# Kernel optimization log

Measured on AMD Instinct MI355X. Metric: run time of the kernel, lower is better.

## Reference

```python
import jax, jax.numpy as jnp
import numpy as np

B, S, D_MODEL = 1, 2048, 2048
H, KVH = 16, 4
HD = D_MODEL // H          # 128
N_REP = H // KVH           # 4 (GQA)
WINDOW = 1024              # window_size=(WINDOW-1, 0): self + 1023 past tokens
CLIP = 8.0
THETA = 500000.0
EPS = 1e-6
SCALE = 1.0 / (HD ** 0.5)


def rms_norm(x, w):
    # per-head RMSNorm over last dim (head_dim)
    var = jnp.mean(jnp.square(x), axis=-1, keepdims=True)
    return x * jax.lax.rsqrt(var + EPS) * w


def rope_tables():
    inv_freq = 1.0 / (THETA ** (jnp.arange(0, HD, 2, dtype=jnp.float32) / HD))
    pos = jnp.arange(S, dtype=jnp.float32)
    freqs = pos[:, None] * inv_freq[None, :]          # [S, HD/2]
    emb = jnp.concatenate([freqs, freqs], axis=-1)    # [S, HD]
    return jnp.cos(emb), jnp.sin(emb)


def rotate_half(x):
    x1, x2 = x[..., : HD // 2], x[..., HD // 2 :]
    return jnp.concatenate([-x2, x1], axis=-1)


def apply_rope(x, cos, sin):
    # x: [B, S, h, HD]; cos/sin: [S, HD]
    return x * cos[None, :, None, :] + rotate_half(x) * sin[None, :, None, :]


def setup_inputs() -> dict:
    key = jax.random.key(0)
    ks = jax.random.split(key, 7)
    w = lambda k, shape: jax.random.normal(k, shape, jnp.float32) * 0.02
    return {
        "x": jax.random.normal(ks[0], (B, S, D_MODEL), jnp.float32),
        "w_q": w(ks[1], (D_MODEL, D_MODEL)),
        "w_k": w(ks[2], (KVH * HD, D_MODEL)),
        "w_v": w(ks[3], (KVH * HD, D_MODEL)),
        "w_out": w(ks[4], (D_MODEL, D_MODEL)),
        "q_norm_w": jnp.ones((HD,), jnp.float32),
        "k_norm_w": jnp.ones((HD,), jnp.float32),
        "sinks": jax.random.normal(ks[5], (H,), jnp.float32),
    }


def reference(x, w_q, w_k, w_v, w_out, q_norm_w, k_norm_w, sinks):
    # fused QKV projection + clip
    q = jnp.clip(x @ w_q.T, -CLIP, CLIP).reshape(B, S, H, HD)
    k = jnp.clip(x @ w_k.T, -CLIP, CLIP).reshape(B, S, KVH, HD)
    v = jnp.clip(x @ w_v.T, -CLIP, CLIP).reshape(B, S, KVH, HD)

    # per-head qk RMSNorm, then RoPE
    q = rms_norm(q, q_norm_w)
    k = rms_norm(k, k_norm_w)
    cos, sin = rope_tables()
    q = apply_rope(q, cos, sin)
    k = apply_rope(k, cos, sin)

    # GQA: repeat_interleave kv heads
    k = jnp.repeat(k, N_REP, axis=2)  # [B, S, H, HD]
    v = jnp.repeat(v, N_REP, axis=2)

    # sliding-window causal attention with a learned per-head sink logit
    logits = jnp.einsum("bqhd,bkhd->bhqk", q, k) * SCALE  # [B, H, S, S]
    qi = jnp.arange(S)[:, None]
    ki = jnp.arange(S)[None, :]
    mask = (ki <= qi) & (ki > qi - WINDOW)                # causal + window
    logits = jnp.where(mask[None, None, :, :], logits, -jnp.inf)

    # sink token: always-visible extra logit sinks[h] with zero value vector
    sink_col = jnp.broadcast_to(sinks[None, :, None, None], (B, H, S, 1))
    full = jnp.concatenate([logits, sink_col], axis=-1)   # [B, H, S, S+1]
    probs = jax.nn.softmax(full, axis=-1)

    att = jnp.einsum("bhqk,bkhd->bqhd", probs[..., :S], v)  # sink value is 0
    return att.reshape(B, S, D_MODEL) @ w_out.T
```

## Files before the change

### kernel.cpp

```cpp
#include <hip/hip_runtime.h>
#include <hip/hip_bf16.h>
#include <math.h>

#define S_LEN 2048
#define DMODEL 2048
#define NH 16
#define NKVH 4
#define HDIM 128
#define WINDOW 1024

typedef __bf16 bf16;
typedef __bf16 bf16x8 __attribute__((ext_vector_type(8)));
typedef __bf16 bf16x4 __attribute__((ext_vector_type(4)));
typedef float floatx4 __attribute__((ext_vector_type(4)));

static __device__ __forceinline__ bf16x8 load_bf8(const bf16* p) {
    return *reinterpret_cast<const bf16x8*>(p);
}

static __device__ __forceinline__ void async16(const bf16* g, bf16* l) {
    __builtin_amdgcn_global_load_lds(
        (const __attribute__((address_space(1))) void*)g,
        (__attribute__((address_space(3))) void*)l, 16, 0, 0);
}

__global__ __launch_bounds__(256) void convert_kernel(
    const float* __restrict__ x, const float* __restrict__ wq,
    const float* __restrict__ wk, const float* __restrict__ wv,
    const float* __restrict__ wo,
    bf16* __restrict__ xb, bf16* __restrict__ wqb, bf16* __restrict__ wkb,
    bf16* __restrict__ wvb, bf16* __restrict__ wob) {
    for (int i = blockIdx.x * blockDim.x + threadIdx.x; i < 3670016;
         i += gridDim.x * blockDim.x) {
        const float* src; bf16* dst; int off;
        if      (i < 1048576) { src = x;  dst = xb;  off = i; }
        else if (i < 2097152) { src = wq; dst = wqb; off = i - 1048576; }
        else if (i < 2359296) { src = wk; dst = wkb; off = i - 2097152; }
        else if (i < 2621440) { src = wv; dst = wvb; off = i - 2359296; }
        else                  { src = wo; dst = wob; off = i - 2621440; }
        float4 v = reinterpret_cast<const float4*>(src)[off];
        union { bf16 b[4]; ushort4 u; } t;
        t.b[0] = (bf16)v.x; t.b[1] = (bf16)v.y;
        t.b[2] = (bf16)v.z; t.b[3] = (bf16)v.w;
        reinterpret_cast<ushort4*>(dst)[off] = t.u;
    }
}

#define GEMM_BODY()                                                            \
    __shared__ __align__(16) bf16 smem[2 * (64 + 128) * 64];        \
    int tid = threadIdx.x;                                                     \
    int lane = tid & 63, wid = tid >> 6;                                       \
    int l15 = lane & 15, quad = lane >> 4;                                     \
    int rlocal = lane >> 3;                                                    \
    int scol = ((lane & 7) ^ rlocal) * 8;                                      \
    const bf16* gA = A + (size_t)(m0 + wid * 16 + rlocal) * K + scol;          \
    const bf16* gB = B + (size_t)(n0 + wid * 32 + rlocal) * K + scol;          \
    int ldsOfA = (wid * 16) * 64;                                               \
    int ldsOfB = (wid * 32) * 64;                                               \
    floatx4 acc[2][4];                                                         \
    _Pragma("unroll") for (int mi = 0; mi < 2; ++mi)                           \
        _Pragma("unroll") for (int ni = 0; ni < 4; ++ni)                       \
            acc[mi][ni] = floatx4{0.f, 0.f, 0.f, 0.f};                         \
    int mb = (wid & 1) * 32, nb = (wid >> 1) * 64;                             \
    _Pragma("unroll") for (int j = 0; j < 2; ++j)                              \
        async16(gA + (size_t)(j * 8) * K, smem + ldsOfA + j * 512);            \
    _Pragma("unroll") for (int j = 0; j < 4; ++j)                              \
        async16(gB + (size_t)(j * 8) * K, smem + 8192 + ldsOfB + j * 512);     \
    int buf = 0;                                                               \
    for (int k0 = 0; k0 < K; k0 += 64) {                                       \
        __syncthreads();                                                       \
        if (k0 + 64 < K) {                                                     \
            int nof = buf ^ 1;                                                 \
            _Pragma("unroll") for (int j = 0; j < 2; ++j)                      \
                async16(gA + (size_t)(j * 8) * K + k0 + 64,                    \
                        smem + nof * 4096 + ldsOfA + j * 512);                 \
            _Pragma("unroll") for (int j = 0; j < 4; ++j)                      \
                async16(gB + (size_t)(j * 8) * K + k0 + 64,                    \
                        smem + 8192 + nof * 8192 + ldsOfB + j * 512);          \
        }                                                                      \
        const bf16* sA = smem + buf * 4096;                                    \
        const bf16* sB = smem + 8192 + buf * 8192;                             \
        _Pragma("unroll") for (int kc = 0; kc < 2; ++kc) {                     \
            bf16x8 af[2], bq[4];                                               \
            int ch = ((kc << 2) + quad) ^ (l15 & 7);                           \
            _Pragma("unroll") for (int i = 0; i < 2; ++i)                      \
                af[i] = load_bf8(sA + (mb + i * 16 + l15) * 64 + ch * 8);      \
            _Pragma("unroll") for (int i = 0; i < 4; ++i)                      \
                bq[i] = load_bf8(sB + (nb + i * 16 + l15) * 64 + ch * 8);      \
            _Pragma("unroll") for (int mi = 0; mi < 2; ++mi)                   \
                _Pragma("unroll") for (int ni = 0; ni < 4; ++ni)               \
                    acc[mi][ni] = __builtin_amdgcn_mfma_f32_16x16x32_bf16(     \
                        af[mi], bq[ni], acc[mi][ni], 0, 0, 0);                 \
        }                                                                      \
        buf ^= 1;                                                              \
    }

__global__ __launch_bounds__(256, 1) void gemm_qkv_fused(
    const bf16* __restrict__ A, const bf16* __restrict__ B,
    const float* __restrict__ qw, const float* __restrict__ kw,
    bf16* __restrict__ qb, bf16* __restrict__ kb, bf16* __restrict__ vtb) {
    const int K = 2048;
    int m0 = blockIdx.y * 128, n0 = blockIdx.x * 256;
    __shared__ __align__(16) bf16 smem[2 * 24576];
    int tid = threadIdx.x;
    int lane = tid & 63, wid = tid >> 6;
    int l15 = lane & 15, quad = lane >> 4;
    int rlocal = lane >> 3;
    int scol = ((lane & 7) ^ rlocal) * 8;
    const bf16* gA = A + (size_t)(m0 + wid * 32 + rlocal) * K + scol;
    const bf16* gB = B + (size_t)(n0 + wid * 64 + rlocal) * K + scol;
    int mb = (wid & 1) * 64, nb = (wid >> 1) * 128;

    floatx4 acc[4][8];
#pragma unroll
    for (int mi = 0; mi < 4; ++mi)
#pragma unroll
        for (int ni = 0; ni < 8; ++ni) acc[mi][ni] = floatx4{0.f, 0.f, 0.f, 0.f};

#pragma unroll
    for (int j = 0; j < 4; ++j)
        async16(gA + (size_t)(j * 8) * K, smem + (wid * 32 + j * 8) * 64);
#pragma unroll
    for (int j = 0; j < 8; ++j)
        async16(gB + (size_t)(j * 8) * K, smem + 8192 + (wid * 64 + j * 8) * 64);

    int buf = 0;
    for (int k0 = 0; k0 < K; k0 += 64) {
        __syncthreads();
        if (k0 + 64 < K) {
            bf16* nbase = smem + (buf ^ 1) * 24576;
#pragma unroll
            for (int j = 0; j < 4; ++j)
                async16(gA + (size_t)(j * 8) * K + k0 + 64,
                        nbase + (wid * 32 + j * 8) * 64);
#pragma unroll
            for (int j = 0; j < 8; ++j)
                async16(gB + (size_t)(j * 8) * K + k0 + 64,
                        nbase + 8192 + (wid * 64 + j * 8) * 64);
        }
        const bf16* sA = smem + buf * 24576;
        const bf16* sB = sA + 8192;
#pragma unroll
        for (int kc = 0; kc < 2; ++kc) {
            bf16x8 af[4], bq[8];
            int ch = ((kc << 2) + quad) ^ (l15 & 7);
#pragma unroll
            for (int i = 0; i < 4; ++i)
                af[i] = load_bf8(sA + (mb + i * 16 + l15) * 64 + ch * 8);
#pragma unroll
            for (int n = 0; n < 8; ++n)
                bq[n] = load_bf8(sB + (nb + n * 16 + l15) * 64 + ch * 8);
#pragma unroll
            for (int mi = 0; mi < 4; ++mi)
#pragma unroll
                for (int ni = 0; ni < 8; ++ni)
                    acc[mi][ni] = __builtin_amdgcn_mfma_f32_16x16x32_bf16(
                        af[mi], bq[ni], acc[mi][ni], 0, 0, 0);
        }
        buf ^= 1;
    }

#pragma unroll
    for (int mi = 0; mi < 4; ++mi)
#pragma unroll
        for (int ni = 0; ni < 8; ++ni)
#pragma unroll
            for (int r = 0; r < 4; ++r)
                acc[mi][ni][r] = fminf(fmaxf(acc[mi][ni][r], -8.0f), 8.0f);

    if (n0 >= 2560) {
#pragma unroll
        for (int mi = 0; mi < 4; ++mi)
#pragma unroll
            for (int ni = 0; ni < 8; ++ni)
#pragma unroll
                for (int r = 0; r < 4; ++r) {
                    int row = m0 + mb + mi * 16 + quad * 4 + r;
                    int n = n0 + nb + ni * 16 + l15;
                    vtb[(size_t)(n - 2560) * 2048 + row] = (bf16)acc[mi][ni][r];
                }
        return;
    }

    const float* nw = (n0 < 2048) ? qw : kw;
    float nwv[8];
#pragma unroll
    for (int ni = 0; ni < 8; ++ni) nwv[ni] = nw[(nb + ni * 16 + l15) & 127];
#pragma unroll
    for (int mi = 0; mi < 4; ++mi)
#pragma unroll
        for (int r = 0; r < 4; ++r) {
            float s = 0.f;
#pragma unroll
            for (int ni = 0; ni < 8; ++ni) s += acc[mi][ni][r] * acc[mi][ni][r];
#pragma unroll
            for (int o = 1; o < 16; o <<= 1) s += __shfl_xor(s, o, 64);
            float rinv = rsqrtf(s * (1.0f / 128.0f) + 1e-6f);
#pragma unroll
            for (int ni = 0; ni < 8; ++ni) acc[mi][ni][r] *= rinv * nwv[ni];
        }

    float invf[4];
#pragma unroll
    for (int ni = 0; ni < 4; ++ni) {
        int fi = ni * 16 + l15;
        invf[ni] = __expf((float)fi * (-13.122363377404328f / 64.0f));
    }
#pragma unroll
    for (int mi = 0; mi < 4; ++mi)
#pragma unroll
        for (int r = 0; r < 4; ++r) {
            int row = mb + mi * 16 + quad * 4 + r;
            int s = m0 + row;
            float pos = (float)s;
#pragma unroll
            for (int ni = 0; ni < 4; ++ni) {
                float ang = pos * invf[ni];
                float c = __cosf(ang), sn = __sinf(ang);
                float a = acc[mi][ni][r], b2 = acc[mi][ni + 4][r];
                float olo = a * c - b2 * sn;
                float ohi = b2 * c + a * sn;
                int nlo = n0 + nb + ni * 16 + l15;
                if (n0 < 2048) {
                    qb[(size_t)s * 2048 + nlo] = (bf16)olo;
                    qb[(size_t)s * 2048 + nlo + 64] = (bf16)ohi;
                } else {
                    kb[(size_t)s * 512 + (nlo - 2048)] = (bf16)olo;
                    kb[(size_t)s * 512 + (nlo - 2048) + 64] = (bf16)ohi;
                }
            }
        }
}

__global__ __launch_bounds__(256) void gemm_out(
    const bf16* __restrict__ A, const bf16* __restrict__ B,
    float* __restrict__ C) {
    const int K = 2048, N = 2048;
    int m0 = blockIdx.y * 64, n0 = blockIdx.x * 128;
    GEMM_BODY()
#pragma unroll
    for (int mi = 0; mi < 2; ++mi)
#pragma unroll
        for (int ni = 0; ni < 4; ++ni)
#pragma unroll
            for (int r = 0; r < 4; ++r) {
                int m = m0 + mb + mi * 16 + quad * 4 + r;
                int n = n0 + nb + ni * 16 + l15;
                C[(size_t)m * N + n] = acc[mi][ni][r];
            }
}

__global__ __launch_bounds__(256) void attn(
    const bf16* __restrict__ qb, const bf16* __restrict__ kb,
    const bf16* __restrict__ vtb, const float* __restrict__ sinks,
    bf16* __restrict__ attb) {
    __shared__ __align__(16) bf16 sK[2][64 * 128];
    __shared__ __align__(16) bf16 sV[2][128 * 64];
    __shared__ __align__(16) bf16 sP[64 * 72];
    __shared__ float redu[64][4];
    int tid = threadIdx.x;
    int lane = tid & 63, wid = tid >> 6;
    int l15 = lane & 15, quad = lane >> 4;
    int h = blockIdx.y, kh = h >> 2;
    int bq0 = blockIdx.x * 64;

    bf16x8 qf[4][4];
#pragma unroll
    for (int ni = 0; ni < 4; ++ni) {
        const bf16* qrow = qb + (size_t)(bq0 + ni * 16 + l15) * 2048 + h * 128 + quad * 8;
#pragma unroll
        for (int kc = 0; kc < 4; ++kc) qf[ni][kc] = load_bf8(qrow + kc * 32);
    }

    floatx4 acc[4][2];
#pragma unroll
    for (int mi = 0; mi < 4; ++mi)
#pragma unroll
        for (int df = 0; df < 2; ++df) acc[mi][df] = floatx4{0.f, 0.f, 0.f, 0.f};
    float lpq[4];
#pragma unroll
    for (int ni = 0; ni < 4; ++ni) lpq[ni] = 0.f;

    int keyit = wid * 4 + (lane >> 4);
    int gcK = (lane & 15) ^ keyit;
    int dimit = wid * 8 + (lane >> 3);
    int gcV = (lane & 7) ^ ((lane >> 3) & 7);

    int tstart = bq0 - 1024; if (tstart < 0) tstart = 0;
    const bf16* kbase = kb + (size_t)kh * 128;
    const bf16* vbase = vtb + (size_t)kh * 128 * 2048;

#pragma unroll
    for (int r = 0; r < 4; ++r) {
        async16(kbase + (size_t)(tstart + r * 16 + keyit) * 512 + gcK * 8,
                sK[0] + (r * 16 + wid * 4) * 128);
        async16(vbase + (size_t)(r * 32 + dimit) * 2048 + tstart + gcV * 8,
                sV[0] + (r * 32 + wid * 8) * 64);
    }

    int buf = 0;
    for (int t = tstart; t <= bq0; t += 64) {
        __syncthreads();
        if (t + 64 <= bq0) {
#pragma unroll
            for (int r = 0; r < 4; ++r) {
                async16(kbase + (size_t)(t + 64 + r * 16 + keyit) * 512 + gcK * 8,
                        sK[buf ^ 1] + (r * 16 + wid * 4) * 128);
                async16(vbase + (size_t)(r * 32 + dimit) * 2048 + t + 64 + gcV * 8,
                        sV[buf ^ 1] + (r * 32 + wid * 8) * 64);
            }
        }
        floatx4 ST[4];
#pragma unroll
        for (int ni = 0; ni < 4; ++ni) ST[ni] = floatx4{0.f, 0.f, 0.f, 0.f};
#pragma unroll
        for (int kc = 0; kc < 4; ++kc) {
            int ch = (kc * 4 + quad) ^ l15;
            bf16x8 kf = load_bf8(sK[buf] + (wid * 16 + l15) * 128 + ch * 8);
#pragma unroll
            for (int ni = 0; ni < 4; ++ni)
                ST[ni] = __builtin_amdgcn_mfma_f32_16x16x32_bf16(kf, qf[ni][kc], ST[ni], 0, 0, 0);
        }
        int kbi = t + wid * 16 + quad * 4;
#pragma unroll
        for (int ni = 0; ni < 4; ++ni) {
            int qi = bq0 + ni * 16 + l15;
            bf16x4 pv;
#pragma unroll
            for (int r = 0; r < 4; ++r) {
                int ki = kbi + r;
                float v = ST[ni][r] * 0.08838834764831845f;
                bool ok = (ki <= qi) && (ki > qi - WINDOW);
                float e = ok ? __expf(v) : 0.0f;
                lpq[ni] += e;
                pv[r] = (bf16)e;
            }
            *(bf16x4*)(sP + (ni * 16 + l15) * 72 + wid * 16 + quad * 4) = pv;
        }
        __syncthreads();
#pragma unroll
        for (int kc = 0; kc < 2; ++kc) {
            bf16x8 pf[4];
#pragma unroll
            for (int mi = 0; mi < 4; ++mi)
                pf[mi] = load_bf8(sP + (mi * 16 + l15) * 72 + kc * 32 + quad * 8);
#pragma unroll
            for (int df = 0; df < 2; ++df) {
                int dim = wid * 32 + df * 16 + l15;
                int ch = (kc * 4 + quad) ^ (l15 & 7);
                bf16x8 vf = load_bf8(sV[buf] + dim * 64 + ch * 8);
#pragma unroll
                for (int mi = 0; mi < 4; ++mi)
                    acc[mi][df] = __builtin_amdgcn_mfma_f32_16x16x32_bf16(pf[mi], vf, acc[mi][df], 0, 0, 0);
            }
        }
        buf ^= 1;
    }

#pragma unroll
    for (int ni = 0; ni < 4; ++ni) {
        float v = lpq[ni];
        v += __shfl_xor(v, 16, 64);
        v += __shfl_xor(v, 32, 64);
        if (quad == 0) redu[ni * 16 + l15][wid] = v;
    }
    __syncthreads();
    float sk = __expf(sinks[h]);
#pragma unroll
    for (int mi = 0; mi < 4; ++mi)
#pragma unroll
        for (int r = 0; r < 4; ++r) {
            int row = mi * 16 + quad * 4 + r;
            float rs = redu[row][0] + redu[row][1] + redu[row][2] + redu[row][3] + sk;
            float inv = 1.0f / rs;
#pragma unroll
            for (int df = 0; df < 2; ++df) {
                int dim = wid * 32 + df * 16 + l15;
                attb[(size_t)(bq0 + row) * 2048 + h * 128 + dim] =
                    (bf16)(acc[mi][df][r] * inv);
            }
        }
}

extern "C" void kernel_launch(void* const* d_in, const int* in_sizes, int n_in,
                              void* d_out, int out_size, void* d_ws, size_t ws_size,
                              hipStream_t stream) {
    const float* x      = (const float*)d_in[0];
    const float* w_q    = (const float*)d_in[1];
    const float* w_k    = (const float*)d_in[2];
    const float* w_v    = (const float*)d_in[3];
    const float* w_out  = (const float*)d_in[4];
    const float* q_norm = (const float*)d_in[5];
    const float* k_norm = (const float*)d_in[6];
    const float* sinks  = (const float*)d_in[7];

    char* ws = (char*)d_ws;
    const size_t MB = 1u << 20;
    bf16* xb   = (bf16*)(ws + 0 * MB);
    bf16* wqb  = (bf16*)(ws + 8 * MB);
    bf16* wkb  = (bf16*)(ws + 16 * MB);
    bf16* wvb  = (bf16*)(ws + 18 * MB);
    bf16* wob  = (bf16*)(ws + 20 * MB);
    bf16* qb   = (bf16*)(ws + 28 * MB);
    bf16* kb   = (bf16*)(ws + 36 * MB);
    bf16* vtb  = (bf16*)(ws + 38 * MB);
    bf16* attb = (bf16*)(ws + 40 * MB);
    bf16* wcomb = wqb;
    float* out = (float*)d_out;

    convert_kernel<<<2048, 256, 0, stream>>>(x, w_q, w_k, w_v, w_out,
                                             xb, wqb, wkb, wvb, wob);
    gemm_qkv_fused<<<dim3(12, 16), 256, 0, stream>>>(xb, wcomb, q_norm, k_norm,
                                                     qb, kb, vtb);
    attn<<<dim3(32, 16), 256, 0, stream>>>(qb, kb, vtb, sinks, attb);
    gemm_out<<<dim3(16, 32), 256, 0, stream>>>(attb, wob, out);
}
```

Before: 202.2 us.

## Triple-buffer GEMM K-loop with explicit vmcnt waits and enlarge out-proj tiles

Both GEMMs move from double-buffered to triple-buffered LDS pipelines. Loads are issued two K-steps ahead, and completion is tracked with explicit s_waitcnt vmcnt counts and a single barrier per iteration instead of a syncthreads-then-load pattern. The output-projection GEMM also grows its tile from 64x128 to 128x128, so it launches 256 blocks instead of 512, with more MFMA per wave. The aim is to hide global-load latency and improve data reuse, at the cost of more LDS per block, fewer blocks for load balance, and correctness that depends on hand-set vmcnt values.

```diff
diff --git a/kernel.cpp b/kernel.cpp
--- a/kernel.cpp
+++ b/kernel.cpp
@@ -46,62 +46,13 @@
     }
 }
 
-#define GEMM_BODY()                                                            \
-    __shared__ __align__(16) bf16 smem[2 * (64 + 128) * 64];        \
-    int tid = threadIdx.x;                                                     \
-    int lane = tid & 63, wid = tid >> 6;                                       \
-    int l15 = lane & 15, quad = lane >> 4;                                     \
-    int rlocal = lane >> 3;                                                    \
-    int scol = ((lane & 7) ^ rlocal) * 8;                                      \
-    const bf16* gA = A + (size_t)(m0 + wid * 16 + rlocal) * K + scol;          \
-    const bf16* gB = B + (size_t)(n0 + wid * 32 + rlocal) * K + scol;          \
-    int ldsOfA = (wid * 16) * 64;                                               \
-    int ldsOfB = (wid * 32) * 64;                                               \
-    floatx4 acc[2][4];                                                         \
-    _Pragma("unroll") for (int mi = 0; mi < 2; ++mi)                           \
-        _Pragma("unroll") for (int ni = 0; ni < 4; ++ni)                       \
-            acc[mi][ni] = floatx4{0.f, 0.f, 0.f, 0.f};                         \
-    int mb = (wid & 1) * 32, nb = (wid >> 1) * 64;                             \
-    _Pragma("unroll") for (int j = 0; j < 2; ++j)                              \
-        async16(gA + (size_t)(j * 8) * K, smem + ldsOfA + j * 512);            \
-    _Pragma("unroll") for (int j = 0; j < 4; ++j)                              \
-        async16(gB + (size_t)(j * 8) * K, smem + 8192 + ldsOfB + j * 512);     \
-    int buf = 0;                                                               \
-    for (int k0 = 0; k0 < K; k0 += 64) {                                       \
-        __syncthreads();                                                       \
-        if (k0 + 64 < K) {                                                     \
-            int nof = buf ^ 1;                                                 \
-            _Pragma("unroll") for (int j = 0; j < 2; ++j)                      \
-                async16(gA + (size_t)(j * 8) * K + k0 + 64,                    \
-                        smem + nof * 4096 + ldsOfA + j * 512);                 \
-            _Pragma("unroll") for (int j = 0; j < 4; ++j)                      \
-                async16(gB + (size_t)(j * 8) * K + k0 + 64,                    \
-                        smem + 8192 + nof * 8192 + ldsOfB + j * 512);          \
-        }                                                                      \
-        const bf16* sA = smem + buf * 4096;                                    \
-        const bf16* sB = smem + 8192 + buf * 8192;                             \
-        _Pragma("unroll") for (int kc = 0; kc < 2; ++kc) {                     \
-            bf16x8 af[2], bq[4];                                               \
-            int ch = ((kc << 2) + quad) ^ (l15 & 7);                           \
-            _Pragma("unroll") for (int i = 0; i < 2; ++i)                      \
-                af[i] = load_bf8(sA + (mb + i * 16 + l15) * 64 + ch * 8);      \
-            _Pragma("unroll") for (int i = 0; i < 4; ++i)                      \
-                bq[i] = load_bf8(sB + (nb + i * 16 + l15) * 64 + ch * 8);      \
-            _Pragma("unroll") for (int mi = 0; mi < 2; ++mi)                   \
-                _Pragma("unroll") for (int ni = 0; ni < 4; ++ni)               \
-                    acc[mi][ni] = __builtin_amdgcn_mfma_f32_16x16x32_bf16(     \
-                        af[mi], bq[ni], acc[mi][ni], 0, 0, 0);                 \
-        }                                                                      \
-        buf ^= 1;                                                              \
-    }
-
 __global__ __launch_bounds__(256, 1) void gemm_qkv_fused(
     const bf16* __restrict__ A, const bf16* __restrict__ B,
     const float* __restrict__ qw, const float* __restrict__ kw,
     bf16* __restrict__ qb, bf16* __restrict__ kb, bf16* __restrict__ vtb) {
     const int K = 2048;
     int m0 = blockIdx.y * 128, n0 = blockIdx.x * 256;
-    __shared__ __align__(16) bf16 smem[2 * 24576];
+    __shared__ __align__(16) bf16 smem[3 * 24576];
     int tid = threadIdx.x;
     int lane = tid & 63, wid = tid >> 6;
     int l15 = lane & 15, quad = lane >> 4;
@@ -118,27 +69,39 @@
         for (int ni = 0; ni < 8; ++ni) acc[mi][ni] = floatx4{0.f, 0.f, 0.f, 0.f};
 
 #pragma unroll
-    for (int j = 0; j < 4; ++j)
-        async16(gA + (size_t)(j * 8) * K, smem + (wid * 32 + j * 8) * 64);
-#pragma unroll
-    for (int j = 0; j < 8; ++j)
-        async16(gB + (size_t)(j * 8) * K, smem + 8192 + (wid * 64 + j * 8) * 64);
-
-    int buf = 0;
-    for (int k0 = 0; k0 < K; k0 += 64) {
-        __syncthreads();
-        if (k0 + 64 < K) {
-            bf16* nbase = smem + (buf ^ 1) * 24576;
+    for (int s = 0; s < 2; ++s) {
+        bf16* dst = smem + s * 24576;
+#pragma unroll
+        for (int j = 0; j < 4; ++j)
+            async16(gA + (size_t)(j * 8) * K + s * 64,
+                    dst + (wid * 32 + j * 8) * 64);
+#pragma unroll
+        for (int j = 0; j < 8; ++j)
+            async16(gB + (size_t)(j * 8) * K + s * 64,
+                    dst + 8192 + (wid * 64 + j * 8) * 64);
+    }
+
+    int slot = 0;
+#pragma unroll 1
+    for (int t = 0; t < 32; ++t) {
+        if (t < 31) asm volatile("s_waitcnt vmcnt(12)" ::: "memory");
+        else        asm volatile("s_waitcnt vmcnt(0)" ::: "memory");
+        __builtin_amdgcn_s_barrier();
+        __builtin_amdgcn_sched_barrier(0);
+        if (t < 30) {
+            int s2 = slot + 2; if (s2 >= 3) s2 -= 3;
+            bf16* dst = smem + s2 * 24576;
+            int kof = (t + 2) * 64;
 #pragma unroll
             for (int j = 0; j < 4; ++j)
-                async16(gA + (size_t)(j * 8) * K + k0 + 64,
-                        nbase + (wid * 32 + j * 8) * 64);
+                async16(gA + (size_t)(j * 8) * K + kof,
+                        dst + (wid * 32 + j * 8) * 64);
 #pragma unroll
             for (int j = 0; j < 8; ++j)
-                async16(gB + (size_t)(j * 8) * K + k0 + 64,
-                        nbase + 8192 + (wid * 64 + j * 8) * 64);
-        }
-        const bf16* sA = smem + buf * 24576;
+                async16(gB + (size_t)(j * 8) * K + kof,
+                        dst + 8192 + (wid * 64 + j * 8) * 64);
+        }
+        const bf16* sA = smem + slot * 24576;
         const bf16* sB = sA + 8192;
 #pragma unroll
         for (int kc = 0; kc < 2; ++kc) {
@@ -157,7 +120,7 @@
                     acc[mi][ni] = __builtin_amdgcn_mfma_f32_16x16x32_bf16(
                         af[mi], bq[ni], acc[mi][ni], 0, 0, 0);
         }
-        buf ^= 1;
+        ++slot; if (slot == 3) slot = 0;
     }
 
 #pragma unroll
@@ -232,14 +195,82 @@
         }
 }
 
-__global__ __launch_bounds__(256) void gemm_out(
+__global__ __launch_bounds__(256, 1) void gemm_out(
     const bf16* __restrict__ A, const bf16* __restrict__ B,
     float* __restrict__ C) {
     const int K = 2048, N = 2048;
-    int m0 = blockIdx.y * 64, n0 = blockIdx.x * 128;
-    GEMM_BODY()
-#pragma unroll
-    for (int mi = 0; mi < 2; ++mi)
+    int m0 = blockIdx.y * 128, n0 = blockIdx.x * 128;
+    __shared__ __align__(16) bf16 smem[3 * 16384];
+    int tid = threadIdx.x;
+    int lane = tid & 63, wid = tid >> 6;
+    int l15 = lane & 15, quad = lane >> 4;
+    int rlocal = lane >> 3;
+    int scol = ((lane & 7) ^ rlocal) * 8;
+    const bf16* gA = A + (size_t)(m0 + wid * 32 + rlocal) * K + scol;
+    const bf16* gB = B + (size_t)(n0 + wid * 32 + rlocal) * K + scol;
+    int mb = (wid & 1) * 64, nb = (wid >> 1) * 64;
+
+    floatx4 acc[4][4];
+#pragma unroll
+    for (int mi = 0; mi < 4; ++mi)
+#pragma unroll
+        for (int ni = 0; ni < 4; ++ni) acc[mi][ni] = floatx4{0.f, 0.f, 0.f, 0.f};
+
+#pragma unroll
+    for (int s = 0; s < 2; ++s) {
+        bf16* dst = smem + s * 16384;
+#pragma unroll
+        for (int j = 0; j < 4; ++j) {
+            async16(gA + (size_t)(j * 8) * K + s * 64,
+                    dst + (wid * 32 + j * 8) * 64);
+            async16(gB + (size_t)(j * 8) * K + s * 64,
+                    dst + 8192 + (wid * 32 + j * 8) * 64);
+        }
+    }
+
+    int slot = 0;
+#pragma unroll 1
+    for (int t = 0; t < 32; ++t) {
+        if (t < 31) asm volatile("s_waitcnt vmcnt(8)" ::: "memory");
+        else        asm volatile("s_waitcnt vmcnt(0)" ::: "memory");
+        __builtin_amdgcn_s_barrier();
+        __builtin_amdgcn_sched_barrier(0);
+        if (t < 30) {
+            int s2 = slot + 2; if (s2 >= 3) s2 -= 3;
+            bf16* dst = smem + s2 * 16384;
+            int kof = (t + 2) * 64;
+#pragma unroll
+            for (int j = 0; j < 4; ++j) {
+                async16(gA + (size_t)(j * 8) * K + kof,
+                        dst + (wid * 32 + j * 8) * 64);
+                async16(gB + (size_t)(j * 8) * K + kof,
+                        dst + 8192 + (wid * 32 + j * 8) * 64);
+            }
+        }
+        const bf16* sA = smem + slot * 16384;
+        const bf16* sB = sA + 8192;
+#pragma unroll
+        for (int kc = 0; kc < 2; ++kc) {
+            bf16x8 af[4], bq[4];
+            int ch = ((kc << 2) + quad) ^ (l15 & 7);
+#pragma unroll
+            for (int i = 0; i < 4; ++i)
+                af[i] = load_bf8(sA + (mb + i * 16 + l15) * 64 + ch * 8);
+#pragma unroll
+            for (int n = 0; n < 4; ++n)
+                bq[n] = load_bf8(sB + (nb + n * 16 + l15) * 64 + ch * 8);
+#pragma unroll
+            for (int mi = 0; mi < 4; ++mi)
+#pragma unroll
+                for (int ni = 0; ni < 4; ++ni)
+                    acc[mi][ni] = __builtin_amdgcn_mfma_f32_16x16x32_bf16(
+                        af[mi], bq[ni], acc[mi][ni], 0, 0, 0);
+        }
+        ++slot; if (slot == 3) slot = 0;
+    }
+
+#pragma unroll
+    for (int mi = 0; mi < 4; ++mi)
 #pragma unroll
         for (int ni = 0; ni < 4; ++ni)
 #pragma unroll
@@ -413,5 +444,5 @@
     gemm_qkv_fused<<<dim3(12, 16), 256, 0, stream>>>(xb, wcomb, q_norm, k_norm,
                                                      qb, kb, vtb);
     attn<<<dim3(32, 16), 256, 0, stream>>>(qb, kb, vtb, sinks, attb);
-    gemm_out<<<dim3(16, 32), 256, 0, stream>>>(attb, wob, out);
-}
+    gemm_out<<<dim3(16, 16), 256, 0, stream>>>(attb, wob, out);
+}
```

Result: slower. 206.5 us (+2.2%).
